# Kernel tuning notes

Hardware: AMD Instinct MI355X
Metric: run time of the kernel (lower is better)

## Reference

```python
import jax, jax.numpy as jnp
import numpy as np

N, C, HID, FEAT = 4096, 1024, 512, 128
KS = (5, 10, 15)  # k values used when k == -1 (hyedge_concat path)


def _sq_cdist(x):
    # squared pairwise euclidean distances; monotone in torch.cdist for topk
    n = (x * x).sum(-1)
    d2 = n[:, None] + n[None, :] - 2.0 * (x @ x.T)
    return jnp.maximum(d2, 0.0)


def neighbor_distance(x, k):
    # k nearest neighbors (smallest distance, self included) -> incidence H [N, N]
    # hyperedge e (column) = neighborhood of node e
    _, idx = jax.lax.top_k(-_sq_cdist(x), k)  # [N, k]
    n = x.shape[0]
    H = jnp.zeros((n, n), x.dtype).at[idx, jnp.arange(n)[:, None]].set(1.0)
    return H


def build_H(x, k):
    if k == -1:  # k is a static Python int
        return jnp.concatenate([neighbor_distance(x, kk) for kk in KS], axis=1)
    return neighbor_distance(x, k)


def hyconv(x, H, W):
    Dv = H.sum(1)  # node degree [N]
    De = H.sum(0)  # edge degree [E]
    dv = jnp.where(Dv > 0, 1.0 / jnp.sqrt(Dv), 0.0)
    de = jnp.where(De > 0, 1.0 / De, 0.0)
    m = (H.T @ (x * dv[:, None])) * de[:, None]  # [E, C]
    return ((H @ m) * dv[:, None]) @ W


def feat_model(x, H, W1, W2):
    return hyconv(jax.nn.relu(hyconv(x, H, W1)), H, W2)


def setup_inputs() -> dict:
    key = jax.random.key(0)
    k1, k2, k3, k4 = jax.random.split(key, 4)
    return {
        "fts_gt": jax.random.normal(k1, (N, C), jnp.float32),
        "fts1": jax.random.normal(k2, (N, C), jnp.float32),
        "W1": jax.random.normal(k3, (C, HID), jnp.float32) / np.sqrt(C).astype(np.float32),
        "W2": jax.random.normal(k4, (HID, FEAT), jnp.float32) / np.sqrt(HID).astype(np.float32),
        "k": -1,
    }


def reference(fts_gt, fts1, W1, W2, k):
    H_gt = build_H(fts_gt, k)
    H1 = build_H(fts1, k)
    feat_gt = feat_model(fts_gt, H_gt, W1, W2)  # [N, FEAT]
    feat1 = feat_model(fts1, H1, W1, W2)
    # sensitive == 'attribute': mean over node dim
    feat_gt = feat_gt.mean(axis=0)
    feat1 = feat1.mean(axis=0)
    y0 = feat_gt.sum()
    y1 = feat1.sum()
    y_compare = (feat_gt[None] - feat1[None]).sum()[None]  # shape [1]
    return (jax.nn.sigmoid(y_compare), y0, y1)
```

## Files before the change

kernel.cpp:

```cpp
#include <hip/hip_runtime.h>
#include <math.h>


#define NN   4096
#define CC   1024
#define HIDN 512
#define FEATN 128
#define NE   12288
#define KTOT 30
#define KMAX 15
#define CH   16
#define MAXCH (NN + NN * KTOT / CH)

typedef __attribute__((ext_vector_type(8))) short bf16x8;
typedef __attribute__((ext_vector_type(4))) float f32x4;
typedef unsigned short ushort_t;

__device__ __forceinline__ unsigned short bf16_rne(float x) {
    unsigned u = __float_as_uint(x);
    unsigned r = (u + 0x7FFFu + ((u >> 16) & 1u)) >> 16;
    return (unsigned short)r;
}
__device__ __forceinline__ float bf16_lo(unsigned u) { return __uint_as_float(u << 16); }
__device__ __forceinline__ float bf16_hi(unsigned u) { return __uint_as_float(u & 0xFFFF0000u); }
__device__ __forceinline__ unsigned packbf(float a, float b) {
    return (unsigned)bf16_rne(a) | ((unsigned)bf16_rne(b) << 16);
}

__device__ __forceinline__ void async16(void* lds, const void* g) {
    __builtin_amdgcn_global_load_lds((const __attribute__((address_space(1))) unsigned int*)g,
                                     (__attribute__((address_space(3))) unsigned int*)lds, 16, 0, 0);
}

__global__ __launch_bounds__(256) void k_rownorm(const float* __restrict__ X,
                                                 float* __restrict__ nrm) {
    __shared__ float s[256];
    int i = blockIdx.x, t = threadIdx.x;
    const float* row = X + (size_t)i * CC;
    float acc = 0.f;
#pragma unroll
    for (int j = 0; j < CC / 256; ++j) { float v = row[t + 256 * j]; acc += v * v; }
    s[t] = acc; __syncthreads();
    for (int d = 128; d > 0; d >>= 1) { if (t < d) s[t] += s[t + d]; __syncthreads(); }
    if (t == 0) nrm[i] = s[0];
}

__global__ __launch_bounds__(256) void k_split(const float* __restrict__ X,
                                               ushort_t* __restrict__ Xh,
                                               ushort_t* __restrict__ Xl) {
    int p = blockIdx.x * 256 + threadIdx.x;
    float4 v = *reinterpret_cast<const float4*>(&X[(size_t)p * 4]);
    float f[4] = { v.x, v.y, v.z, v.w };
    ushort4 H, L;
    unsigned short hh[4], ll[4];
#pragma unroll
    for (int i = 0; i < 4; ++i) {
        unsigned short hb = bf16_rne(f[i]);
        float hf = __uint_as_float((unsigned)hb << 16);
        hh[i] = hb;
        ll[i] = bf16_rne(f[i] - hf);
    }
    H.x = hh[0]; H.y = hh[1]; H.z = hh[2]; H.w = hh[3];
    L.x = ll[0]; L.y = ll[1]; L.z = ll[2]; L.w = ll[3];
    *reinterpret_cast<ushort4*>(&Xh[(size_t)p * 4]) = H;
    *reinterpret_cast<ushort4*>(&Xl[(size_t)p * 4]) = L;
}

__global__ __launch_bounds__(256) void k_wt(const float* __restrict__ W,
                                            ushort_t* __restrict__ Th,
                                            ushort_t* __restrict__ Tl) {
    __shared__ float s[32][33];
    int bx = blockIdx.x, by = blockIdx.y;
    int tx = threadIdx.x & 31, ty = threadIdx.x >> 5;
#pragma unroll
    for (int rr = 0; rr < 4; ++rr) {
        int k = by * 32 + ty + rr * 8;
        s[ty + rr * 8][tx] = W[(size_t)k * HIDN + bx * 32 + tx];
    }
    __syncthreads();
#pragma unroll
    for (int rr = 0; rr < 4; ++rr) {
        int n = bx * 32 + ty + rr * 8;
        int k = by * 32 + tx;
        float x = s[tx][ty + rr * 8];
        unsigned short hb = bf16_rne(x);
        Th[(size_t)n * CC + k] = hb;
        Tl[(size_t)n * CC + k] = bf16_rne(x - __uint_as_float((unsigned)hb << 16));
    }
}

__global__ __launch_bounds__(256) void k_w2bar(const float* __restrict__ W2,
                                               float* __restrict__ wbar) {
    int k = blockIdx.x * 256 + threadIdx.x;
    const float* row = W2 + (size_t)k * FEATN;
    float s = 0.f;
#pragma unroll
    for (int f = 0; f < FEATN; f += 4) {
        float4 v = *reinterpret_cast<const float4*>(&row[f]);
        s += v.x + v.y + v.z + v.w;
    }
    wbar[k] = s;
}

template <bool SYM, bool SCALE, bool OUTB>
__global__ __launch_bounds__(256) void k_mm(const ushort_t* __restrict__ Ah,
                                            const ushort_t* __restrict__ Al,
                                            const ushort_t* __restrict__ Bth,
                                            const ushort_t* __restrict__ Btl,
                                            const float* __restrict__ rowscale,
                                            float* __restrict__ C,
                                            ushort_t* __restrict__ Cb, int ldc) {
    int bi, bj;
    if (SYM) {
        int b0 = (int)blockIdx.x;
        int L = (b0 & 7) * 66 + (b0 >> 3);
        int rem = L, si = 0;
        for (; si < 8; ++si) {
            int grp = 10 + (7 - si) * 16;
            if (rem < grp) break;
            rem -= grp;
        }
        int sj, u, v;
        if (rem < 10) {
            int uu = 0, r2 = rem;
            while (r2 >= 4 - uu) { r2 -= 4 - uu; ++uu; }
            u = uu; v = uu + r2; sj = si;
        } else {
            int r2 = rem - 10;
            sj = si + 1 + (r2 >> 4);
            int w2 = r2 & 15;
            u = w2 >> 2; v = w2 & 3;
        }
        bi = si * 4 + u; bj = sj * 4 + v;
    } else {
        bi = blockIdx.y; bj = blockIdx.x;
    }
    __shared__ ushort_t lds[4][128][64];
    int t = threadIdx.x;
    int w = t >> 6, l = t & 63;
    int wr = (w >> 1) * 64, wc = (w & 1) * 64;

    f32x4 acc[4][4];
#pragma unroll
    for (int i = 0; i < 4; ++i)
#pragma unroll
        for (int j = 0; j < 4; ++j) acc[i][j] = (f32x4){0.f, 0.f, 0.f, 0.f};

    const ushort_t* src[4] = {
        Ah  + (size_t)bi * 128 * 1024,
        Al  + (size_t)bi * 128 * 1024,
        Bth + (size_t)bj * 128 * 1024,
        Btl + (size_t)bj * 128 * 1024
    };
    int rloc8 = l >> 3;
    int sp = l & 7;
    int sl = sp ^ rloc8;

    for (int kt = 0; kt < 16; ++kt) {
        int k0 = kt * 64;
#pragma unroll
        for (int q = 0; q < 4; ++q) {
#pragma unroll
            for (int s = 0; s < 4; ++s) {
                int rbase = (w * 4 + s) * 8;
                const ushort_t* g = src[q] + (size_t)(rbase + rloc8) * 1024 + k0 + sl * 8;
                async16(&lds[q][rbase][0], g);
            }
        }
        __syncthreads();
#pragma unroll
        for (int ks = 0; ks < 2; ++ks) {
            bf16x8 ah[4], al[4], bh[4], bl[4];
            int kg = ks * 4 + (l >> 4);
#pragma unroll
            for (int mi = 0; mi < 4; ++mi) {
                int row = wr + mi * 16 + (l & 15);
                int ph = kg ^ (row & 7);
                ah[mi] = *reinterpret_cast<const bf16x8*>(&lds[0][row][ph * 8]);
                al[mi] = *reinterpret_cast<const bf16x8*>(&lds[1][row][ph * 8]);
            }
#pragma unroll
            for (int nj = 0; nj < 4; ++nj) {
                int row = wc + nj * 16 + (l & 15);
                int ph = kg ^ (row & 7);
                bh[nj] = *reinterpret_cast<const bf16x8*>(&lds[2][row][ph * 8]);
                bl[nj] = *reinterpret_cast<const bf16x8*>(&lds[3][row][ph * 8]);
            }
#pragma unroll
            for (int mi = 0; mi < 4; ++mi)
#pragma unroll
                for (int nj = 0; nj < 4; ++nj) {
                    acc[mi][nj] = __builtin_amdgcn_mfma_f32_16x16x32_bf16(ah[mi], bh[nj], acc[mi][nj], 0, 0, 0);
                    acc[mi][nj] = __builtin_amdgcn_mfma_f32_16x16x32_bf16(ah[mi], bl[nj], acc[mi][nj], 0, 0, 0);
                    acc[mi][nj] = __builtin_amdgcn_mfma_f32_16x16x32_bf16(al[mi], bh[nj], acc[mi][nj], 0, 0, 0);
                }
        }
        __syncthreads();
    }
    if (!OUTB) {
#pragma unroll
        for (int mi = 0; mi < 4; ++mi) {
#pragma unroll
            for (int r = 0; r < 4; ++r) {
                int rg = bi * 128 + wr + mi * 16 + (l >> 4) * 4 + r;
                float sc = SCALE ? rowscale[rg] : 1.0f;
#pragma unroll
                for (int nj = 0; nj < 4; ++nj) {
                    int cg = bj * 128 + wc + nj * 16 + (l & 15);
                    C[(size_t)rg * ldc + cg] = acc[mi][nj][r] * sc;
                }
            }
        }
        if (SYM && bi != bj) {
            float* fl = (float*)lds;
#pragma unroll
            for (int mi = 0; mi < 4; ++mi)
#pragma unroll
                for (int r = 0; r < 4; ++r) {
                    int rl = wr + mi * 16 + (l >> 4) * 4 + r;
#pragma unroll
                    for (int nj = 0; nj < 4; ++nj) {
                        int cl = wc + nj * 16 + (l & 15);
                        fl[cl * 128 + rl] = acc[mi][nj][r];
                    }
                }
            __syncthreads();
            int row = t >> 1, co = (t & 1) * 64;
            const float4* srow = reinterpret_cast<const float4*>(&fl[row * 128 + co]);
            float4* dst = reinterpret_cast<float4*>(&C[(size_t)(bj * 128 + row) * ldc + bi * 128 + co]);
#pragma unroll
            for (int q = 0; q < 16; ++q) dst[q] = srow[q];
        }
    } else {
#pragma unroll
        for (int mi = 0; mi < 4; ++mi) {
#pragma unroll
            for (int r = 0; r < 4; ++r) {
                int rg = bi * 128 + wr + mi * 16 + (l >> 4) * 4 + r;
                float sc = SCALE ? rowscale[rg] : 1.0f;
#pragma unroll
                for (int nj = 0; nj < 4; ++nj) {
                    int cg = bj * 128 + wc + nj * 16 + (l & 15);
                    Cb[(size_t)rg * ldc + cg] = bf16_rne(acc[mi][nj][r] * sc);
                }
            }
        }
    }
}

__global__ __launch_bounds__(256) void k_topk(const float* __restrict__ G,
                                              const float* __restrict__ nrm,
                                              int* __restrict__ idx_out) {
    __shared__ unsigned long long wsm[4];
    int e = blockIdx.x, t = threadIdx.x;
    float ne = nrm[e];
    const float* Grow = G + (size_t)e * NN;
    unsigned long long key[16];
    unsigned long long my = ~0ull;
#pragma unroll
    for (int j = 0; j < 16; ++j) {
        int i = t + 256 * j;
        float v = fmaxf(ne + nrm[i] - 2.0f * Grow[i], 0.0f);
        unsigned long long k = ((unsigned long long)__float_as_uint(v) << 32) | (unsigned)i;
        key[j] = k;
        my = k < my ? k : my;
    }
    for (int r = 0; r < KMAX; ++r) {
        unsigned long long m = my;
#pragma unroll
        for (int d = 1; d < 64; d <<= 1) {
            unsigned long long o = __shfl_xor(m, d);
            m = o < m ? o : m;
        }
        if ((t & 63) == 0) wsm[t >> 6] = m;
        __syncthreads();
        unsigned long long b0 = wsm[0] < wsm[1] ? wsm[0] : wsm[1];
        unsigned long long b1 = wsm[2] < wsm[3] ? wsm[2] : wsm[3];
        unsigned long long bk = b0 < b1 ? b0 : b1;
        int win = (int)(unsigned)bk;
        if (t == 0) idx_out[e * 16 + r] = win;
        if (t == (win & 255)) {
            int jw = win >> 8;
#pragma unroll
            for (int jj = 0; jj < 16; ++jj) if (jj == jw) key[jj] = ~0ull;
            my = ~0ull;
#pragma unroll
            for (int jj = 0; jj < 16; ++jj) my = key[jj] < my ? key[jj] : my;
        }
        __syncthreads();
    }
}

__device__ __forceinline__ void decode_pair(int p, int& e, int& b, int& j) {
    e = p / KTOT;
    int q = p - e * KTOT;
    if (q < 5)       { b = 0; j = q; }
    else if (q < 15) { b = 1; j = q - 5; }
    else             { b = 2; j = q - 15; }
}

__global__ __launch_bounds__(256) void k_count(const int* __restrict__ idx, int* __restrict__ Dv) {
    int p = blockIdx.x * 256 + threadIdx.x;
    int e, b, j; decode_pair(p, e, b, j);
    (void)b;
    atomicAdd(&Dv[idx[e * 16 + j]], 1);
}

__global__ __launch_bounds__(256) void k_dv(const int* __restrict__ Dv, float* __restrict__ dvv) {
    int i = blockIdx.x * 256 + threadIdx.x;
    int d = Dv[i];
    dvv[i] = d > 0 ? 1.0f / sqrtf((float)d) : 0.0f;
}

__global__ __launch_bounds__(1024) void k_scan(const int* __restrict__ Dv,
                                               int* __restrict__ offs,
                                               int* __restrict__ cur,
                                               int* __restrict__ chunkoffs,
                                               int* __restrict__ nchunks) {
    __shared__ int s[1024];
    int t = threadIdx.x;
    int v[4]; int sum = 0;
#pragma unroll
    for (int j = 0; j < 4; ++j) { v[j] = Dv[t * 4 + j]; sum += v[j]; }
    s[t] = sum; __syncthreads();
    for (int d = 1; d < 1024; d <<= 1) {
        int add = (t >= d) ? s[t - d] : 0;
        __syncthreads();
        s[t] += add;
        __syncthreads();
    }
    int run = s[t] - sum;
#pragma unroll
    for (int j = 0; j < 4; ++j) { offs[t * 4 + j] = run; cur[t * 4 + j] = run; run += v[j]; }
    if (t == 1023) offs[NN] = run;
    __syncthreads();
    int c[4]; int csum = 0;
#pragma unroll
    for (int j = 0; j < 4; ++j) { c[j] = (v[j] + CH - 1) / CH; csum += c[j]; }
    s[t] = csum; __syncthreads();
    for (int d = 1; d < 1024; d <<= 1) {
        int add = (t >= d) ? s[t - d] : 0;
        __syncthreads();
        s[t] += add;
        __syncthreads();
    }
    int crun = s[t] - csum;
#pragma unroll
    for (int j = 0; j < 4; ++j) { chunkoffs[t * 4 + j] = crun; crun += c[j]; }
    if (t == 1023) { chunkoffs[NN] = crun; *nchunks = crun; }
}

__global__ __launch_bounds__(256) void k_fill(const int* __restrict__ idx,
                                              int* __restrict__ cur,
                                              int* __restrict__ adj) {
    int p = blockIdx.x * 256 + threadIdx.x;
    int e, b, j; decode_pair(p, e, b, j);
    int i = idx[e * 16 + j];
    int eg = b * NN + e;
    int pos = atomicAdd(&cur[i], 1);
    adj[pos] = eg;
}

__global__ __launch_bounds__(256) void k_tasks(const int* __restrict__ chunkoffs,
                                               int* __restrict__ task_node) {
    int i = blockIdx.x * 256 + threadIdx.x;
    int c0 = chunkoffs[i], c1 = chunkoffs[i + 1];
    for (int c = c0; c < c1; ++c) task_node[c] = i;
}

__global__ __launch_bounds__(256) void k_ze(const int* __restrict__ idx,
                                            const float* __restrict__ dvv,
                                            float* __restrict__ ze) {
    int eg = blockIdx.x * 256 + threadIdx.x;
    int b = eg >> 12, e = eg & (NN - 1);
    int kb = (b == 0) ? 5 : (b == 1) ? 10 : 15;
    const int* row = idx + e * 16;
    float s = 0.f;
    for (int j = 0; j < kb; ++j) s += dvv[row[j]];
    ze[eg] = s / (float)kb;
}

__global__ __launch_bounds__(256) void k_ascat(const int* __restrict__ idx,
                                               const float* __restrict__ ze,
                                               float* __restrict__ a) {
    int p = blockIdx.x * 256 + threadIdx.x;
    int e, b, j; decode_pair(p, e, b, j);
    atomicAdd(&a[idx[e * 16 + j]], ze[b * NN + e]);
}

__global__ __launch_bounds__(256) void k_edge3(const int* __restrict__ idx,
                                               const ushort_t* __restrict__ t1b,
                                               ushort_t* __restrict__ m) {
    int p = blockIdx.x * 256 + threadIdx.x;
    int e = p >> 6;
    int c8 = (p & 63) * 8;
    const int* row = idx + e * 16;
    float acc[8] = {};
    auto addrow = [&](int j) {
        uint4 raw = *reinterpret_cast<const uint4*>(&t1b[(size_t)row[j] * HIDN + c8]);
        acc[0] += bf16_lo(raw.x); acc[1] += bf16_hi(raw.x);
        acc[2] += bf16_lo(raw.y); acc[3] += bf16_hi(raw.y);
        acc[4] += bf16_lo(raw.z); acc[5] += bf16_hi(raw.z);
        acc[6] += bf16_lo(raw.w); acc[7] += bf16_hi(raw.w);
    };
    auto store = [&](size_t eg, float sc) {
        uint4 o;
        o.x = packbf(acc[0] * sc, acc[1] * sc);
        o.y = packbf(acc[2] * sc, acc[3] * sc);
        o.z = packbf(acc[4] * sc, acc[5] * sc);
        o.w = packbf(acc[6] * sc, acc[7] * sc);
        *reinterpret_cast<uint4*>(&m[eg * HIDN + c8]) = o;
    };
#pragma unroll
    for (int j = 0; j < 5; ++j) addrow(j);
    store((size_t)e, 0.2f);
#pragma unroll
    for (int j = 5; j < 10; ++j) addrow(j);
    store((size_t)(NN + e), 0.1f);
#pragma unroll
    for (int j = 10; j < 15; ++j) addrow(j);
    store((size_t)(2 * NN + e), 1.0f / 15.0f);
}

__global__ __launch_bounds__(256) void k_chunk(const int* __restrict__ offs,
                                               const int* __restrict__ chunkoffs,
                                               const int* __restrict__ task_node,
                                               const int* __restrict__ nchunks,
                                               const int* __restrict__ adj,
                                               const ushort_t* __restrict__ m,
                                               float* __restrict__ partial) {
    int task = blockIdx.x * 4 + threadIdx.x / 64;
    if (task >= *nchunks) return;
    int c8 = (threadIdx.x & 63) * 8;
    int i = task_node[task];
    int ck = task - chunkoffs[i];
    int q0 = offs[i] + ck * CH;
    int n = offs[i + 1] - q0;
    n = n < CH ? n : CH;
    int e[CH];
#pragma unroll
    for (int j = 0; j < CH; ++j) e[j] = (j < n) ? adj[q0 + j] : -1;
    float acc[8] = {};
#pragma unroll
    for (int j = 0; j < CH; ++j) {
        if (e[j] >= 0) {
            uint4 raw = *reinterpret_cast<const uint4*>(&m[(size_t)e[j] * HIDN + c8]);
            acc[0] += bf16_lo(raw.x); acc[1] += bf16_hi(raw.x);
            acc[2] += bf16_lo(raw.y); acc[3] += bf16_hi(raw.y);
            acc[4] += bf16_lo(raw.z); acc[5] += bf16_hi(raw.z);
            acc[6] += bf16_lo(raw.w); acc[7] += bf16_hi(raw.w);
        }
    }
    float* o = &partial[(size_t)task * HIDN + c8];
    *reinterpret_cast<float4*>(o)     = make_float4(acc[0], acc[1], acc[2], acc[3]);
    *reinterpret_cast<float4*>(o + 4) = make_float4(acc[4], acc[5], acc[6], acc[7]);
}

__global__ __launch_bounds__(256) void k_comb2(const int* __restrict__ chunkoffs,
                                               const float* __restrict__ dvv,
                                               const float* __restrict__ a,
                                               const float* __restrict__ wbar,
                                               const float* __restrict__ partial,
                                               float* __restrict__ g) {
    __shared__ float s[256];
    int p = blockIdx.x * 256 + threadIdx.x;
    int i = p >> 7;
    int c4 = (p & 127) * 4;
    int c0 = chunkoffs[i], c1 = chunkoffs[i + 1];
    float4 acc = make_float4(0.f, 0.f, 0.f, 0.f);
    for (int c = c0; c < c1; ++c) {
        float4 v = *reinterpret_cast<const float4*>(&partial[(size_t)c * HIDN + c4]);
        acc.x += v.x; acc.y += v.y; acc.z += v.z; acc.w += v.w;
    }
    float dv = dvv[i];
    float4 wv = *reinterpret_cast<const float4*>(&wbar[c4]);
    float val = fmaxf(acc.x * dv, 0.f) * wv.x + fmaxf(acc.y * dv, 0.f) * wv.y +
                fmaxf(acc.z * dv, 0.f) * wv.z + fmaxf(acc.w * dv, 0.f) * wv.w;
    int t = threadIdx.x;
    s[t] = val; __syncthreads();
    for (int d = 64; d > 0; d >>= 1) {
        if ((t & 127) < d) s[t] += s[t + d];
        __syncthreads();
    }
    if ((t & 127) == 0) g[i] = s[t] * dv * a[i];
}

__global__ __launch_bounds__(1024) void k_yred(const float* __restrict__ g,
                                               float* __restrict__ ys, int slot) {
    __shared__ float s[1024];
    int t = threadIdx.x;
    s[t] = g[t] + g[t + 1024] + g[t + 2048] + g[t + 3072];
    __syncthreads();
    for (int d = 512; d > 0; d >>= 1) { if (t < d) s[t] += s[t + d]; __syncthreads(); }
    if (t == 0) ys[slot] = s[0];
}

__global__ void k_fin(const float* __restrict__ ys, float* __restrict__ out) {
    float y0 = ys[0] / (float)NN, y1 = ys[1] / (float)NN;
    out[0] = 1.0f / (1.0f + expf(-(y0 - y1)));
    out[1] = y0;
    out[2] = y1;
}

extern "C" void kernel_launch(void* const* d_in, const int* in_sizes, int n_in,
                              void* d_out, int out_size, void* d_ws, size_t ws_size,
                              hipStream_t stream) {
    const float* fts[2] = { (const float*)d_in[0], (const float*)d_in[1] };
    const float* W1 = (const float*)d_in[2];
    const float* W2 = (const float*)d_in[3];
    float* out = (float*)d_out;

    char* p = (char*)d_ws;
    auto alloc = [&](size_t b) { char* r = p; p += (b + 255) & ~(size_t)255; return r; };
    float* G    = (float*)alloc((size_t)NN * NN * 4);
    float* nrm  = (float*)alloc((size_t)NN * 4);
    int*   idx  = (int*)  alloc((size_t)NN * 16 * 4);
    int*   Dv   = (int*)  alloc((size_t)NN * 4);
    float* dvv  = (float*)alloc((size_t)NN * 4);
    int*   offs = (int*)  alloc((size_t)(NN + 1) * 4);
    int*   cur  = (int*)  alloc((size_t)NN * 4);
    int*   coffs= (int*)  alloc((size_t)(NN + 1) * 4);
    int*   nch  = (int*)  alloc(4);
    int*   tnode= (int*)  alloc((size_t)MAXCH * 4);
    int*   adj  = (int*)  alloc((size_t)NN * KTOT * 4);
    ushort_t* t1b = (ushort_t*)alloc((size_t)NN * HIDN * 2);
    ushort_t* m   = (ushort_t*)alloc((size_t)NE * HIDN * 2);
    ushort_t* Xh  = (ushort_t*)alloc((size_t)NN * CC * 2);
    ushort_t* Xl  = (ushort_t*)alloc((size_t)NN * CC * 2);
    ushort_t* W1Th = (ushort_t*)alloc((size_t)HIDN * CC * 2);
    ushort_t* W1Tl = (ushort_t*)alloc((size_t)HIDN * CC * 2);
    float* wbar = (float*)alloc((size_t)HIDN * 4);
    float* ze   = (float*)alloc((size_t)NE * 4);
    float* a    = (float*)alloc((size_t)NN * 4);
    float* g    = (float*)alloc((size_t)NN * 4);
    float* ys   = (float*)alloc(2 * 4);

    float* partial = G;

    k_wt<<<dim3(HIDN / 32, CC / 32), 256, 0, stream>>>(W1, W1Th, W1Tl);
    k_w2bar<<<HIDN / 256, 256, 0, stream>>>(W2, wbar);

    for (int s = 0; s < 2; ++s) {
        const float* X = fts[s];
        k_rownorm<<<NN, 256, 0, stream>>>(X, nrm);
        k_split<<<NN * CC / 4 / 256, 256, 0, stream>>>(X, Xh, Xl);
        k_mm<true, false, false><<<528, 256, 0, stream>>>(Xh, Xl, Xh, Xl, nullptr, G, nullptr, NN);
        k_topk<<<NN, 256, 0, stream>>>(G, nrm, idx);
        hipMemsetAsync(Dv, 0, NN * 4, stream);
        k_count<<<NN * KTOT / 256, 256, 0, stream>>>(idx, Dv);
        k_dv<<<NN / 256, 256, 0, stream>>>(Dv, dvv);
        k_scan<<<1, 1024, 0, stream>>>(Dv, offs, cur, coffs, nch);
        k_fill<<<NN * KTOT / 256, 256, 0, stream>>>(idx, cur, adj);
        k_tasks<<<NN / 256, 256, 0, stream>>>(coffs, tnode);
        k_ze<<<NE / 256, 256, 0, stream>>>(idx, dvv, ze);
        hipMemsetAsync(a, 0, NN * 4, stream);
        k_ascat<<<NN * KTOT / 256, 256, 0, stream>>>(idx, ze, a);
        k_mm<false, true, true><<<dim3(HIDN / 128, NN / 128), 256, 0, stream>>>(Xh, Xl, W1Th, W1Tl, dvv, nullptr, t1b, HIDN);
        k_edge3<<<NN * 64 / 256, 256, 0, stream>>>(idx, t1b, m);
        k_chunk<<<(MAXCH + 3) / 4, 256, 0, stream>>>(offs, coffs, tnode, nch, adj, m, partial);
        k_comb2<<<NN * 128 / 256, 256, 0, stream>>>(coffs, dvv, a, wbar, partial, g);
        k_yred<<<1, 1024, 0, stream>>>(g, ys, s);
    }
    k_fin<<<1, 1, 0, stream>>>(ys, out);
}
```

Measured before the change: 691.4 us.

## Switch split-bf16 GEMMs to split-int8 MFMA and fuse CSR build into one kernel

Replaces the bf16 hi/lo split GEMMs (Gram matrix and X·W1) with per-row/per-column scaled int8 hi/lo quantization using i32 16x16x64 MFMA, which halves operand bytes and doubles MFMA k-depth per instruction. It also merges the count/dv/scan/fill/tasks/ze/ascat kernels into a single one-block k_csr kernel that uses LDS atomics, removing many launches and memsets. The symmetric transpose store now goes through a padded LDS tile. The int8 two-level quantization gives roughly 15-bit precision, which risks changing the top-k neighbor choices. The single-block CSR kernel serializes work that previously ran across many blocks.

```diff
diff --git a/kernel.cpp b/kernel.cpp
--- a/kernel.cpp
+++ b/kernel.cpp
@@ -12,8 +12,7 @@
 #define CH   16
 #define MAXCH (NN + NN * KTOT / CH)
 
-typedef __attribute__((ext_vector_type(8))) short bf16x8;
-typedef __attribute__((ext_vector_type(4))) float f32x4;
+typedef __attribute__((ext_vector_type(4))) int i32x4;
 typedef unsigned short ushort_t;
 
 __device__ __forceinline__ unsigned short bf16_rne(float x) {
@@ -32,43 +31,70 @@
                                      (__attribute__((address_space(3))) unsigned int*)lds, 16, 0, 0);
 }
 
-__global__ __launch_bounds__(256) void k_rownorm(const float* __restrict__ X,
-                                                 float* __restrict__ nrm) {
+__global__ __launch_bounds__(256) void k_rownorm2(const float* __restrict__ X,
+                                                  float* __restrict__ nrm,
+                                                  float* __restrict__ qs) {
     __shared__ float s[256];
+    __shared__ float sm[256];
     int i = blockIdx.x, t = threadIdx.x;
     const float* row = X + (size_t)i * CC;
-    float acc = 0.f;
-#pragma unroll
-    for (int j = 0; j < CC / 256; ++j) { float v = row[t + 256 * j]; acc += v * v; }
-    s[t] = acc; __syncthreads();
-    for (int d = 128; d > 0; d >>= 1) { if (t < d) s[t] += s[t + d]; __syncthreads(); }
-    if (t == 0) nrm[i] = s[0];
-}
-
-__global__ __launch_bounds__(256) void k_split(const float* __restrict__ X,
-                                               ushort_t* __restrict__ Xh,
-                                               ushort_t* __restrict__ Xl) {
+    float acc = 0.f, mx = 0.f;
+#pragma unroll
+    for (int j = 0; j < CC / 256; ++j) {
+        float v = row[t + 256 * j];
+        acc += v * v;
+        mx = fmaxf(mx, fabsf(v));
+    }
+    s[t] = acc; sm[t] = mx; __syncthreads();
+    for (int d = 128; d > 0; d >>= 1) {
+        if (t < d) { s[t] += s[t + d]; sm[t] = fmaxf(sm[t], sm[t + d]); }
+        __syncthreads();
+    }
+    if (t == 0) { nrm[i] = s[0]; qs[i] = fmaxf(sm[0], 1e-20f) / 127.0f; }
+}
+
+__global__ __launch_bounds__(256) void k_quant(const float* __restrict__ X,
+                                               const float* __restrict__ qs,
+                                               signed char* __restrict__ H,
+                                               signed char* __restrict__ L) {
     int p = blockIdx.x * 256 + threadIdx.x;
+    int i = p >> 8;
+    float inv = 1.0f / qs[i];
     float4 v = *reinterpret_cast<const float4*>(&X[(size_t)p * 4]);
     float f[4] = { v.x, v.y, v.z, v.w };
-    ushort4 H, L;
-    unsigned short hh[4], ll[4];
-#pragma unroll
-    for (int i = 0; i < 4; ++i) {
-        unsigned short hb = bf16_rne(f[i]);
-        float hf = __uint_as_float((unsigned)hb << 16);
-        hh[i] = hb;
-        ll[i] = bf16_rne(f[i] - hf);
-    }
-    H.x = hh[0]; H.y = hh[1]; H.z = hh[2]; H.w = hh[3];
-    L.x = ll[0]; L.y = ll[1]; L.z = ll[2]; L.w = ll[3];
-    *reinterpret_cast<ushort4*>(&Xh[(size_t)p * 4]) = H;
-    *reinterpret_cast<ushort4*>(&Xl[(size_t)p * 4]) = L;
-}
-
-__global__ __launch_bounds__(256) void k_wt(const float* __restrict__ W,
-                                            ushort_t* __restrict__ Th,
-                                            ushort_t* __restrict__ Tl) {
+    char hh[4], ll[4];
+#pragma unroll
+    for (int j = 0; j < 4; ++j) {
+        float xs = f[j] * inv;
+        float h = rintf(xs);
+        float l = rintf((xs - h) * 128.0f);
+        hh[j] = (char)(int)h;
+        ll[j] = (char)(int)l;
+    }
+    *reinterpret_cast<char4*>(&H[(size_t)p * 4]) = make_char4(hh[0], hh[1], hh[2], hh[3]);
+    *reinterpret_cast<char4*>(&L[(size_t)p * 4]) = make_char4(ll[0], ll[1], ll[2], ll[3]);
+}
+
+__global__ __launch_bounds__(256) void k_w1max(const float* __restrict__ W,
+                                               float* __restrict__ sig) {
+    __shared__ float s[256];
+    int t = threadIdx.x;
+    int col = blockIdx.x * 64 + (t & 63);
+    int seg = t >> 6;
+    float mx = 0.f;
+    for (int k = seg * 256; k < seg * 256 + 256; ++k)
+        mx = fmaxf(mx, fabsf(W[(size_t)k * HIDN + col]));
+    s[t] = mx; __syncthreads();
+    if (seg == 0) {
+        mx = fmaxf(fmaxf(s[t], s[t + 64]), fmaxf(s[t + 128], s[t + 192]));
+        sig[col] = fmaxf(mx, 1e-20f) / 127.0f;
+    }
+}
+
+__global__ __launch_bounds__(256) void k_wt8(const float* __restrict__ W,
+                                             const float* __restrict__ sig,
+                                             signed char* __restrict__ Th,
+                                             signed char* __restrict__ Tl) {
     __shared__ float s[32][33];
     int bx = blockIdx.x, by = blockIdx.y;
     int tx = threadIdx.x & 31, ty = threadIdx.x >> 5;
@@ -83,9 +109,11 @@
         int n = bx * 32 + ty + rr * 8;
         int k = by * 32 + tx;
         float x = s[tx][ty + rr * 8];
-        unsigned short hb = bf16_rne(x);
-        Th[(size_t)n * CC + k] = hb;
-        Tl[(size_t)n * CC + k] = bf16_rne(x - __uint_as_float((unsigned)hb << 16));
+        float xs = x / sig[n];
+        float h = rintf(xs);
+        float l = rintf((xs - h) * 128.0f);
+        Th[(size_t)n * CC + k] = (char)(int)h;
+        Tl[(size_t)n * CC + k] = (char)(int)l;
     }
 }
 
@@ -102,14 +130,15 @@
     wbar[k] = s;
 }
 
-template <bool SYM, bool SCALE, bool OUTB>
-__global__ __launch_bounds__(256) void k_mm(const ushort_t* __restrict__ Ah,
-                                            const ushort_t* __restrict__ Al,
-                                            const ushort_t* __restrict__ Bth,
-                                            const ushort_t* __restrict__ Btl,
-                                            const float* __restrict__ rowscale,
-                                            float* __restrict__ C,
-                                            ushort_t* __restrict__ Cb, int ldc) {
+template <bool SYM, bool OUTB>
+__global__ __launch_bounds__(256) void k_mm8(const signed char* __restrict__ Ah,
+                                             const signed char* __restrict__ Al,
+                                             const signed char* __restrict__ Bh,
+                                             const signed char* __restrict__ Bl,
+                                             const float* __restrict__ rs,
+                                             const float* __restrict__ cs,
+                                             float* __restrict__ C,
+                                             ushort_t* __restrict__ Cb, int ldc) {
     int bi, bj;
     if (SYM) {
         int b0 = (int)blockIdx.x;
@@ -135,115 +164,98 @@
     } else {
         bi = blockIdx.y; bj = blockIdx.x;
     }
-    __shared__ ushort_t lds[4][128][64];
+    __shared__ char smem[SYM ? 128 * 129 * 4 : 4 * 128 * 64];
+    char (*lds)[128][64] = reinterpret_cast<char(*)[128][64]>(smem);
     int t = threadIdx.x;
     int w = t >> 6, l = t & 63;
     int wr = (w >> 1) * 64, wc = (w & 1) * 64;
 
-    f32x4 acc[4][4];
+    i32x4 acc1[4][4], acc2[4][4];
 #pragma unroll
     for (int i = 0; i < 4; ++i)
 #pragma unroll
-        for (int j = 0; j < 4; ++j) acc[i][j] = (f32x4){0.f, 0.f, 0.f, 0.f};
-
-    const ushort_t* src[4] = {
-        Ah  + (size_t)bi * 128 * 1024,
-        Al  + (size_t)bi * 128 * 1024,
-        Bth + (size_t)bj * 128 * 1024,
-        Btl + (size_t)bj * 128 * 1024
+        for (int j = 0; j < 4; ++j) { acc1[i][j] = (i32x4){0,0,0,0}; acc2[i][j] = (i32x4){0,0,0,0}; }
+
+    const signed char* src[4] = {
+        Ah + (size_t)bi * 128 * 1024,
+        Al + (size_t)bi * 128 * 1024,
+        Bh + (size_t)bj * 128 * 1024,
+        Bl + (size_t)bj * 128 * 1024
     };
-    int rloc8 = l >> 3;
-    int sp = l & 7;
-    int sl = sp ^ rloc8;
+    int srow = l >> 2;
+    int sslot = (l & 3) ^ ((l >> 3) & 3);
+
+    int col = l & 15;
+    int kg = l >> 4;
 
     for (int kt = 0; kt < 16; ++kt) {
         int k0 = kt * 64;
 #pragma unroll
         for (int q = 0; q < 4; ++q) {
 #pragma unroll
-            for (int s = 0; s < 4; ++s) {
-                int rbase = (w * 4 + s) * 8;
-                const ushort_t* g = src[q] + (size_t)(rbase + rloc8) * 1024 + k0 + sl * 8;
+            for (int s2 = 0; s2 < 2; ++s2) {
+                int rbase = (w * 2 + s2) * 16;
+                const signed char* g = src[q] + (size_t)(rbase + srow) * 1024 + k0 + sslot * 16;
                 async16(&lds[q][rbase][0], g);
             }
         }
         __syncthreads();
-#pragma unroll
-        for (int ks = 0; ks < 2; ++ks) {
-            bf16x8 ah[4], al[4], bh[4], bl[4];
-            int kg = ks * 4 + (l >> 4);
-#pragma unroll
-            for (int mi = 0; mi < 4; ++mi) {
-                int row = wr + mi * 16 + (l & 15);
-                int ph = kg ^ (row & 7);
-                ah[mi] = *reinterpret_cast<const bf16x8*>(&lds[0][row][ph * 8]);
-                al[mi] = *reinterpret_cast<const bf16x8*>(&lds[1][row][ph * 8]);
+        i32x4 ah[4], al4[4], bh4[4], bl4[4];
+#pragma unroll
+        for (int mi = 0; mi < 4; ++mi) {
+            int row = wr + mi * 16 + col;
+            int ph = kg ^ ((row >> 1) & 3);
+            ah[mi]  = *reinterpret_cast<const i32x4*>(&lds[0][row][ph * 16]);
+            al4[mi] = *reinterpret_cast<const i32x4*>(&lds[1][row][ph * 16]);
+        }
+#pragma unroll
+        for (int nj = 0; nj < 4; ++nj) {
+            int row = wc + nj * 16 + col;
+            int ph = kg ^ ((row >> 1) & 3);
+            bh4[nj] = *reinterpret_cast<const i32x4*>(&lds[2][row][ph * 16]);
+            bl4[nj] = *reinterpret_cast<const i32x4*>(&lds[3][row][ph * 16]);
+        }
+#pragma unroll
+        for (int mi = 0; mi < 4; ++mi)
+#pragma unroll
+            for (int nj = 0; nj < 4; ++nj) {
+                acc1[mi][nj] = __builtin_amdgcn_mfma_i32_16x16x64_i8(ah[mi], bh4[nj], acc1[mi][nj], 0, 0, 0);
+                acc2[mi][nj] = __builtin_amdgcn_mfma_i32_16x16x64_i8(ah[mi], bl4[nj], acc2[mi][nj], 0, 0, 0);
+                acc2[mi][nj] = __builtin_amdgcn_mfma_i32_16x16x64_i8(al4[mi], bh4[nj], acc2[mi][nj], 0, 0, 0);
             }
+        __syncthreads();
+    }
+
+    float* fl = reinterpret_cast<float*>(smem);
+#pragma unroll
+    for (int mi = 0; mi < 4; ++mi) {
+#pragma unroll
+        for (int r = 0; r < 4; ++r) {
+            int rl = wr + mi * 16 + (l >> 4) * 4 + r;
+            int rg = bi * 128 + rl;
+            float rsv = rs[rg];
 #pragma unroll
             for (int nj = 0; nj < 4; ++nj) {
-                int row = wc + nj * 16 + (l & 15);
-                int ph = kg ^ (row & 7);
-                bh[nj] = *reinterpret_cast<const bf16x8*>(&lds[2][row][ph * 8]);
-                bl[nj] = *reinterpret_cast<const bf16x8*>(&lds[3][row][ph * 8]);
-            }
-#pragma unroll
-            for (int mi = 0; mi < 4; ++mi)
-#pragma unroll
-                for (int nj = 0; nj < 4; ++nj) {
-                    acc[mi][nj] = __builtin_amdgcn_mfma_f32_16x16x32_bf16(ah[mi], bh[nj], acc[mi][nj], 0, 0, 0);
-                    acc[mi][nj] = __builtin_amdgcn_mfma_f32_16x16x32_bf16(ah[mi], bl[nj], acc[mi][nj], 0, 0, 0);
-                    acc[mi][nj] = __builtin_amdgcn_mfma_f32_16x16x32_bf16(al[mi], bh[nj], acc[mi][nj], 0, 0, 0);
-                }
-        }
-        __syncthreads();
-    }
-    if (!OUTB) {
-#pragma unroll
-        for (int mi = 0; mi < 4; ++mi) {
-#pragma unroll
-            for (int r = 0; r < 4; ++r) {
-                int rg = bi * 128 + wr + mi * 16 + (l >> 4) * 4 + r;
-                float sc = SCALE ? rowscale[rg] : 1.0f;
-#pragma unroll
-                for (int nj = 0; nj < 4; ++nj) {
-                    int cg = bj * 128 + wc + nj * 16 + (l & 15);
-                    C[(size_t)rg * ldc + cg] = acc[mi][nj][r] * sc;
+                int cl = wc + nj * 16 + col;
+                int cg = bj * 128 + cl;
+                float v = ((float)acc1[mi][nj][r] + (float)acc2[mi][nj][r] * (1.0f / 128.0f))
+                          * rsv * cs[cg];
+                if (OUTB) {
+                    Cb[(size_t)rg * ldc + cg] = bf16_rne(v);
+                } else {
+                    C[(size_t)rg * ldc + cg] = v;
+                    if (SYM && bi != bj) fl[cl * 129 + rl] = v;
                 }
             }
         }
-        if (SYM && bi != bj) {
-            float* fl = (float*)lds;
-#pragma unroll
-            for (int mi = 0; mi < 4; ++mi)
-#pragma unroll
-                for (int r = 0; r < 4; ++r) {
-                    int rl = wr + mi * 16 + (l >> 4) * 4 + r;
-#pragma unroll
-                    for (int nj = 0; nj < 4; ++nj) {
-                        int cl = wc + nj * 16 + (l & 15);
-                        fl[cl * 128 + rl] = acc[mi][nj][r];
-                    }
-                }
-            __syncthreads();
-            int row = t >> 1, co = (t & 1) * 64;
-            const float4* srow = reinterpret_cast<const float4*>(&fl[row * 128 + co]);
-            float4* dst = reinterpret_cast<float4*>(&C[(size_t)(bj * 128 + row) * ldc + bi * 128 + co]);
-#pragma unroll
-            for (int q = 0; q < 16; ++q) dst[q] = srow[q];
-        }
-    } else {
-#pragma unroll
-        for (int mi = 0; mi < 4; ++mi) {
-#pragma unroll
-            for (int r = 0; r < 4; ++r) {
-                int rg = bi * 128 + wr + mi * 16 + (l >> 4) * 4 + r;
-                float sc = SCALE ? rowscale[rg] : 1.0f;
-#pragma unroll
-                for (int nj = 0; nj < 4; ++nj) {
-                    int cg = bj * 128 + wc + nj * 16 + (l & 15);
-                    Cb[(size_t)rg * ldc + cg] = bf16_rne(acc[mi][nj][r] * sc);
-                }
-            }
+    }
+    if (SYM && !OUTB && bi != bj) {
+        __syncthreads();
+#pragma unroll 4
+        for (int it = 0; it < 64; ++it) {
+            int row = it * 2 + (t >> 7);
+            int c2 = t & 127;
+            C[(size_t)(bj * 128 + row) * ldc + bi * 128 + c2] = fl[row * 129 + c2];
         }
     }
 }
@@ -299,93 +311,90 @@
     else             { b = 2; j = q - 15; }
 }
 
-__global__ __launch_bounds__(256) void k_count(const int* __restrict__ idx, int* __restrict__ Dv) {
-    int p = blockIdx.x * 256 + threadIdx.x;
-    int e, b, j; decode_pair(p, e, b, j);
-    (void)b;
-    atomicAdd(&Dv[idx[e * 16 + j]], 1);
-}
-
-__global__ __launch_bounds__(256) void k_dv(const int* __restrict__ Dv, float* __restrict__ dvv) {
-    int i = blockIdx.x * 256 + threadIdx.x;
-    int d = Dv[i];
-    dvv[i] = d > 0 ? 1.0f / sqrtf((float)d) : 0.0f;
-}
-
-__global__ __launch_bounds__(1024) void k_scan(const int* __restrict__ Dv,
-                                               int* __restrict__ offs,
-                                               int* __restrict__ cur,
-                                               int* __restrict__ chunkoffs,
-                                               int* __restrict__ nchunks) {
-    __shared__ int s[1024];
+__global__ __launch_bounds__(1024) void k_csr(const int* __restrict__ idx,
+                                              const float* __restrict__ qs,
+                                              float* __restrict__ dvv,
+                                              float* __restrict__ rs1,
+                                              int* __restrict__ offs,
+                                              int* __restrict__ coffs,
+                                              int* __restrict__ nch,
+                                              int* __restrict__ tnode,
+                                              int* __restrict__ adj,
+                                              float* __restrict__ ze,
+                                              float* __restrict__ a) {
+    __shared__ int cnt[NN];
+    __shared__ int sb[1024];
     int t = threadIdx.x;
+    for (int i = t; i < NN; i += 1024) cnt[i] = 0;
+    __syncthreads();
+    for (int p = t; p < NN * KTOT; p += 1024) {
+        int e, b, j; decode_pair(p, e, b, j); (void)b;
+        atomicAdd(&cnt[idx[e * 16 + j]], 1);
+    }
+    __syncthreads();
     int v[4]; int sum = 0;
 #pragma unroll
-    for (int j = 0; j < 4; ++j) { v[j] = Dv[t * 4 + j]; sum += v[j]; }
-    s[t] = sum; __syncthreads();
+    for (int j = 0; j < 4; ++j) { v[j] = cnt[t * 4 + j]; sum += v[j]; }
+#pragma unroll
+    for (int j = 0; j < 4; ++j) {
+        int i = t * 4 + j;
+        float dv = v[j] > 0 ? 1.0f / sqrtf((float)v[j]) : 0.0f;
+        dvv[i] = dv;
+        rs1[i] = dv * qs[i];
+    }
+    __syncthreads();
+    sb[t] = sum; __syncthreads();
     for (int d = 1; d < 1024; d <<= 1) {
-        int add = (t >= d) ? s[t - d] : 0;
-        __syncthreads();
-        s[t] += add;
-        __syncthreads();
-    }
-    int run = s[t] - sum;
-#pragma unroll
-    for (int j = 0; j < 4; ++j) { offs[t * 4 + j] = run; cur[t * 4 + j] = run; run += v[j]; }
+        int add = (t >= d) ? sb[t - d] : 0;
+        __syncthreads(); sb[t] += add; __syncthreads();
+    }
+    int run = sb[t] - sum;
+#pragma unroll
+    for (int j = 0; j < 4; ++j) { offs[t * 4 + j] = run; cnt[t * 4 + j] = run; run += v[j]; }
     if (t == 1023) offs[NN] = run;
     __syncthreads();
     int c[4]; int csum = 0;
 #pragma unroll
     for (int j = 0; j < 4; ++j) { c[j] = (v[j] + CH - 1) / CH; csum += c[j]; }
-    s[t] = csum; __syncthreads();
+    sb[t] = csum; __syncthreads();
     for (int d = 1; d < 1024; d <<= 1) {
-        int add = (t >= d) ? s[t - d] : 0;
-        __syncthreads();
-        s[t] += add;
-        __syncthreads();
-    }
-    int crun = s[t] - csum;
-#pragma unroll
-    for (int j = 0; j < 4; ++j) { chunkoffs[t * 4 + j] = crun; crun += c[j]; }
-    if (t == 1023) { chunkoffs[NN] = crun; *nchunks = crun; }
-}
-
-__global__ __launch_bounds__(256) void k_fill(const int* __restrict__ idx,
-                                              int* __restrict__ cur,
-                                              int* __restrict__ adj) {
-    int p = blockIdx.x * 256 + threadIdx.x;
-    int e, b, j; decode_pair(p, e, b, j);
-    int i = idx[e * 16 + j];
-    int eg = b * NN + e;
-    int pos = atomicAdd(&cur[i], 1);
-    adj[pos] = eg;
-}
-
-__global__ __launch_bounds__(256) void k_tasks(const int* __restrict__ chunkoffs,
-                                               int* __restrict__ task_node) {
-    int i = blockIdx.x * 256 + threadIdx.x;
-    int c0 = chunkoffs[i], c1 = chunkoffs[i + 1];
-    for (int c = c0; c < c1; ++c) task_node[c] = i;
-}
-
-__global__ __launch_bounds__(256) void k_ze(const int* __restrict__ idx,
-                                            const float* __restrict__ dvv,
-                                            float* __restrict__ ze) {
-    int eg = blockIdx.x * 256 + threadIdx.x;
-    int b = eg >> 12, e = eg & (NN - 1);
-    int kb = (b == 0) ? 5 : (b == 1) ? 10 : 15;
-    const int* row = idx + e * 16;
-    float s = 0.f;
-    for (int j = 0; j < kb; ++j) s += dvv[row[j]];
-    ze[eg] = s / (float)kb;
-}
-
-__global__ __launch_bounds__(256) void k_ascat(const int* __restrict__ idx,
-                                               const float* __restrict__ ze,
-                                               float* __restrict__ a) {
-    int p = blockIdx.x * 256 + threadIdx.x;
-    int e, b, j; decode_pair(p, e, b, j);
-    atomicAdd(&a[idx[e * 16 + j]], ze[b * NN + e]);
+        int add = (t >= d) ? sb[t - d] : 0;
+        __syncthreads(); sb[t] += add; __syncthreads();
+    }
+    int crun = sb[t] - csum;
+#pragma unroll
+    for (int j = 0; j < 4; ++j) {
+        coffs[t * 4 + j] = crun;
+        for (int q = 0; q < c[j]; ++q) tnode[crun + q] = t * 4 + j;
+        crun += c[j];
+    }
+    if (t == 1023) { coffs[NN] = crun; *nch = crun; }
+    __syncthreads();
+    for (int p = t; p < NN * KTOT; p += 1024) {
+        int e, b, j; decode_pair(p, e, b, j);
+        int i = idx[e * 16 + j];
+        int pos = atomicAdd(&cnt[i], 1);
+        adj[pos] = b * NN + e;
+    }
+    __syncthreads();
+    for (int eg = t; eg < NE; eg += 1024) {
+        int b = eg >> 12, e = eg & (NN - 1);
+        int kb = (b == 0) ? 5 : (b == 1) ? 10 : 15;
+        const int* row = idx + e * 16;
+        float s = 0.f;
+        for (int j = 0; j < kb; ++j) s += dvv[row[j]];
+        ze[eg] = s / (float)kb;
+    }
+    __syncthreads();
+    float* af = (float*)cnt;
+    for (int i = t; i < NN; i += 1024) af[i] = 0.f;
+    __syncthreads();
+    for (int p = t; p < NN * KTOT; p += 1024) {
+        int e, b, j; decode_pair(p, e, b, j);
+        atomicAdd(&af[idx[e * 16 + j]], ze[b * NN + e]);
+    }
+    __syncthreads();
+    for (int i = t; i < NN; i += 1024) a[i] = af[i];
 }
 
 __global__ __launch_bounds__(256) void k_edge3(const int* __restrict__ idx,
@@ -514,21 +523,22 @@
     auto alloc = [&](size_t b) { char* r = p; p += (b + 255) & ~(size_t)255; return r; };
     float* G    = (float*)alloc((size_t)NN * NN * 4);
     float* nrm  = (float*)alloc((size_t)NN * 4);
+    float* qs   = (float*)alloc((size_t)NN * 4);
     int*   idx  = (int*)  alloc((size_t)NN * 16 * 4);
-    int*   Dv   = (int*)  alloc((size_t)NN * 4);
     float* dvv  = (float*)alloc((size_t)NN * 4);
+    float* rs1  = (float*)alloc((size_t)NN * 4);
     int*   offs = (int*)  alloc((size_t)(NN + 1) * 4);
-    int*   cur  = (int*)  alloc((size_t)NN * 4);
     int*   coffs= (int*)  alloc((size_t)(NN + 1) * 4);
     int*   nch  = (int*)  alloc(4);
     int*   tnode= (int*)  alloc((size_t)MAXCH * 4);
     int*   adj  = (int*)  alloc((size_t)NN * KTOT * 4);
+    signed char* Xqh = (signed char*)alloc((size_t)NN * CC);
+    signed char* Xql = (signed char*)alloc((size_t)NN * CC);
+    signed char* Wqh = (signed char*)alloc((size_t)HIDN * CC);
+    signed char* Wql = (signed char*)alloc((size_t)HIDN * CC);
+    float* w1sig = (float*)alloc((size_t)HIDN * 4);
     ushort_t* t1b = (ushort_t*)alloc((size_t)NN * HIDN * 2);
     ushort_t* m   = (ushort_t*)alloc((size_t)NE * HIDN * 2);
-    ushort_t* Xh  = (ushort_t*)alloc((size_t)NN * CC * 2);
-    ushort_t* Xl  = (ushort_t*)alloc((size_t)NN * CC * 2);
-    ushort_t* W1Th = (ushort_t*)alloc((size_t)HIDN * CC * 2);
-    ushort_t* W1Tl = (ushort_t*)alloc((size_t)HIDN * CC * 2);
     float* wbar = (float*)alloc((size_t)HIDN * 4);
     float* ze   = (float*)alloc((size_t)NE * 4);
     float* a    = (float*)alloc((size_t)NN * 4);
@@ -537,25 +547,18 @@
 
     float* partial = G;
 
-    k_wt<<<dim3(HIDN / 32, CC / 32), 256, 0, stream>>>(W1, W1Th, W1Tl);
+    k_w1max<<<HIDN / 64, 256, 0, stream>>>(W1, w1sig);
+    k_wt8<<<dim3(HIDN / 32, CC / 32), 256, 0, stream>>>(W1, w1sig, Wqh, Wql);
     k_w2bar<<<HIDN / 256, 256, 0, stream>>>(W2, wbar);
 
     for (int s = 0; s < 2; ++s) {
         const float* X = fts[s];
-        k_rownorm<<<NN, 256, 0, stream>>>(X, nrm);
-        k_split<<<NN * CC / 4 / 256, 256, 0, stream>>>(X, Xh, Xl);
-        k_mm<true, false, false><<<528, 256, 0, stream>>>(Xh, Xl, Xh, Xl, nullptr, G, nullptr, NN);
+        k_rownorm2<<<NN, 256, 0, stream>>>(X, nrm, qs);
+        k_quant<<<NN * CC / 4 / 256, 256, 0, stream>>>(X, qs, Xqh, Xql);
+        k_mm8<true, false><<<528, 256, 0, stream>>>(Xqh, Xql, Xqh, Xql, qs, qs, G, nullptr, NN);
         k_topk<<<NN, 256, 0, stream>>>(G, nrm, idx);
-        hipMemsetAsync(Dv, 0, NN * 4, stream);
-        k_count<<<NN * KTOT / 256, 256, 0, stream>>>(idx, Dv);
-        k_dv<<<NN / 256, 256, 0, stream>>>(Dv, dvv);
-        k_scan<<<1, 1024, 0, stream>>>(Dv, offs, cur, coffs, nch);
-        k_fill<<<NN * KTOT / 256, 256, 0, stream>>>(idx, cur, adj);
-        k_tasks<<<NN / 256, 256, 0, stream>>>(coffs, tnode);
-        k_ze<<<NE / 256, 256, 0, stream>>>(idx, dvv, ze);
-        hipMemsetAsync(a, 0, NN * 4, stream);
-        k_ascat<<<NN * KTOT / 256, 256, 0, stream>>>(idx, ze, a);
-        k_mm<false, true, true><<<dim3(HIDN / 128, NN / 128), 256, 0, stream>>>(Xh, Xl, W1Th, W1Tl, dvv, nullptr, t1b, HIDN);
+        k_csr<<<1, 1024, 0, stream>>>(idx, qs, dvv, rs1, offs, coffs, nch, tnode, adj, ze, a);
+        k_mm8<false, true><<<dim3(HIDN / 128, NN / 128), 256, 0, stream>>>(Xqh, Xql, Wqh, Wql, rs1, w1sig, nullptr, t1b, HIDN);
         k_edge3<<<NN * 64 / 256, 256, 0, stream>>>(idx, t1b, m);
         k_chunk<<<(MAXCH + 3) / 4, 256, 0, stream>>>(offs, coffs, tnode, nch, adj, m, partial);
         k_comb2<<<NN * 128 / 256, 256, 0, stream>>>(coffs, dvv, a, wbar, partial, g);
```

Result: slower. 1.186 ms (+71.5%).
